# Kernel tuning notes

Measured on AMD Instinct MI355X. Metric: run time of the kernel, lower is better.

Reference implementation:

```python
import jax, jax.numpy as jnp
import numpy as np

EPS = 1e-8
B, N, K, UNITS, FDIMS = 4, 20000, 8, 64, 64
S = K + 1

def _norm(x):
    # euclidean norm over last axis with safe (zero) gradient at 0, same forward as tf.norm
    s = jnp.sum(x * x, axis=-1, keepdims=True)
    return jnp.where(s == 0, 0.0, jnp.sqrt(jnp.where(s == 0, 1.0, s)))

def _conv1d(x, w, b):
    # x: (B,N,S,Cin), w: (3,Cin,Cout); keras Conv1D(kernel=3, padding='same') over the S (1+K) axis + relu
    Bx, Nx, Sx, C = x.shape
    y = jax.lax.conv_general_dilated(x.reshape(Bx * Nx, Sx, C), w, (1,), 'SAME',
                                     dimension_numbers=('NWC', 'WIO', 'NWC'))
    return jax.nn.relu(y + b).reshape(Bx, Nx, Sx, -1)

def _encode(x, ws, bs):
    # encode() from source: channel-sum residual pre-add, then residual loop
    r = _conv1d(x + jnp.sum(x, -1, keepdims=True), ws[0], bs[0])
    for w, b in zip(ws[1:], bs[1:]):
        r = r + _conv1d(r + jnp.sum(r, -1, keepdims=True), w, b)
    return r

def setup_inputs():
    key = jax.random.key(0)
    ks = jax.random.split(key, 32)
    it = iter(list(ks))
    def w(shape, k):
        fan_in = shape[-2] * (shape[0] if len(shape) == 3 else 1)
        return (jax.random.normal(k, shape, jnp.float32) / np.float32(np.sqrt(fan_in)))
    inp = {
        'pc': jax.random.normal(next(it), (B, N, S, 4), jnp.float32),
        'feats': jax.random.normal(next(it), (B, N, S, FDIMS), jnp.float32),
    }
    for name, cin in (('pos', 2), ('rel', 2), ('nrm', 1), ('ang', 3)):
        inp[name + '_w0'] = w((3, cin, UNITS), next(it)); inp[name + '_b0'] = jnp.zeros((UNITS,), jnp.float32)
        inp[name + '_w1'] = w((3, UNITS, UNITS), next(it)); inp[name + '_b1'] = jnp.zeros((UNITS,), jnp.float32)
        inp[name + '_w2'] = w((3, UNITS, UNITS), next(it)); inp[name + '_b2'] = jnp.zeros((UNITS,), jnp.float32)
    inp['mlp_w'] = w((2 * UNITS, UNITS), next(it)); inp['mlp_b'] = jnp.zeros((UNITS,), jnp.float32)
    return inp

def reference(pc, feats, pos_w0, pos_b0, pos_w1, pos_b1, pos_w2, pos_b2,
              rel_w0, rel_b0, rel_w1, rel_b1, rel_w2, rel_b2,
              nrm_w0, nrm_b0, nrm_w1, nrm_b1, nrm_w2, nrm_b2,
              ang_w0, ang_b0, ang_w1, ang_b1, ang_w2, ang_b2,
              mlp_w, mlp_b):
    current = pc[:, :, :1]                          # (B,N,1,4)
    diff = current[..., :2] - pc[..., :2]           # (B,N,S,2)
    norms = _norm(pc[..., :2])                      # (B,N,S,1)
    diff_norm = _norm(diff)
    current_norm = _norm(current)                   # norm over all 4 channels, as in source
    num = jnp.sum(diff * current[..., 2:4], axis=-1, keepdims=True)
    den = diff_norm * current_norm + EPS
    angles = 1.0 - jnp.abs(num / den)
    rppe = jnp.concatenate([pc, diff, norms, angles], axis=-1)  # (B,N,S,8)
    pos, rel_pos = rppe[..., :2], rppe[..., 2:4]
    nrm_in, ang_in = rppe[..., 4:5], rppe[..., 5:]  # faithful to source slicing
    pos_e = _encode(pos, [pos_w0, pos_w1, pos_w2], [pos_b0, pos_b1, pos_b2])
    rel_e = _encode(rel_pos, [rel_w0, rel_w1, rel_w2], [rel_b0, rel_b1, rel_b2])
    nrm_e = _encode(nrm_in, [nrm_w0, nrm_w1, nrm_w2], [nrm_b0, nrm_b1, nrm_b2])
    ang_e = _encode(ang_in, [ang_w0, ang_w1, ang_w2], [ang_b0, ang_b1, ang_b2])
    _ = (pos_e, rel_e)  # computed in the source graph but not used in the output
    r = jax.nn.relu(jnp.einsum('bnsc,co->bnso', jnp.concatenate([nrm_e, ang_e], -1), mlp_w) + mlp_b)
    return jnp.concatenate([r, feats], axis=-1)     # (B,N,S,UNITS+FDIMS)
```

## Files before the change

kernel.cpp:

```cpp
#include <hip/hip_runtime.h>

typedef _Float16 f16;
typedef f16 half4 __attribute__((ext_vector_type(4)));
typedef f16 half8 __attribute__((ext_vector_type(8)));
typedef float f32x4 __attribute__((ext_vector_type(4)));

#define Pv 80000
#define G 7
#define AST 72
#define NROW (G*10+1)
#define NGRP 11429


__global__ void setup_frags(const float* __restrict__ aw0, const float* __restrict__ nw0,
                            const float* __restrict__ aw1, const float* __restrict__ aw2,
                            const float* __restrict__ nw1, const float* __restrict__ nw2,
                            const float* __restrict__ mlp_w, f16* __restrict__ ws)
{
  int tid = blockIdx.x*blockDim.x + threadIdx.x;
  if (tid < 7168){
    int L    = tid / 1792;
    int rem  = tid % 1792;
    int q    = (rem % 448) / 64;
    int lane = rem % 64;
    int nt   = rem / 448;
    const float* W = (L==0)?aw1:(L==1)?aw2:(L==2)?nw1:nw2;
    int n = nt*16 + (lane & 15);
    f16 o8[8];
    #pragma unroll
    for (int j=0;j<8;j++){
      int k = q*32 + (lane>>4)*8 + j;
      float v = 0.f;
      if (k < 192) v = W[k*64 + n];
      else if (k < 195){ int tap = k-192; float s=0.f;
        for (int c=0;c<64;c++) s += W[(tap*64+c)*64 + n]; v = s; }
      o8[j] = (f16)v;
    }
    *(half8*)(ws + (size_t)tid*8) = *(half8*)o8;
  } else if (tid < 8192){
    int t2 = tid - 7168;
    int lane = t2 % 64;
    int q    = (t2 / 64) % 4;
    int nt   = t2 / 256;
    int n = nt*16 + (lane & 15);
    f16 o8[8];
    #pragma unroll
    for (int j=0;j<8;j++){
      int k = q*32 + (lane>>4)*8 + j;
      o8[j] = (f16)mlp_w[k*64 + n];
    }
    *(half8*)(ws + 57344 + (size_t)t2*8) = *(half8*)o8;
  } else if (tid < 8704){
    int t3   = tid - 8192;
    int lane = t3 & 63;
    int nt   = (t3 >> 6) & 3;
    bool isang = t3 < 256;
    int n  = nt*16 + (lane & 15);
    int qd = lane >> 4;
    f16 o8[8];
    #pragma unroll
    for (int j=0;j<8;j++){
      int k = qd*8 + j;
      float v = 0.f;
      if (isang){
        if (k < 9){ int tap = k/3, c = k%3;
          float s3 = aw0[(tap*3+0)*64+n] + aw0[(tap*3+1)*64+n] + aw0[(tap*3+2)*64+n];
          v = aw0[(tap*3+c)*64+n] + s3; }
      } else {
        if (k < 3) v = 2.f * nw0[k*64+n];
      }
      o8[j] = (f16)v;
    }
    *(half8*)(ws + (isang ? 65536 : 67584) + ((size_t)(nt*64+lane))*8) = *(half8*)o8;
  }
}

template<bool IS_ANG>
__device__ __forceinline__ void layer0_mfma(const f16* __restrict__ frag,
    const float* __restrict__ bias, f16* A, int lane, int h, half4 (&cres)[2][4])
{
  const int lo = lane & 15, qd = lane >> 4;
  float bn[4];
  #pragma unroll
  for (int nt=0;nt<4;nt++) bn[nt] = bias[nt*16 + lo];
  f32x4 acc[2][4];
  #pragma unroll
  for (int tt=0;tt<2;tt++)
    #pragma unroll
    for (int nt=0;nt<4;nt++) acc[tt][nt] = (f32x4){bn[nt],bn[nt],bn[nt],bn[nt]};

  half8 bv[4];
  #pragma unroll
  for (int nt=0;nt<4;nt++) bv[nt] = *(const half8*)(frag + ((nt*64+lane))*8);

  const f16 Z = (f16)0;
  #pragma unroll
  for (int tt=0;tt<2;tt++){
    int m = (2*h+tt)*16 + lo; if (m > 62) m = 62;
    int p = m/9, s = m - 9*p;
    const f16* ibp = A + (p*10 + s)*AST + 68;
    half4 h0 = *(const half4*)(ibp);
    half4 h1 = *(const half4*)(ibp + AST);
    half4 h2 = *(const half4*)(ibp + 2*AST);
    half8 av = (half8){Z,Z,Z,Z,Z,Z,Z,Z};
    if (IS_ANG){
      if (qd == 0)      av = (half8){h0[1],h0[2],h0[3],h1[1],h1[2],h1[3],h2[1],h2[2]};
      else if (qd == 1) av = (half8){h2[3],Z,Z,Z,Z,Z,Z,Z};
    } else {
      if (qd == 0)      av = (half8){h0[0],h1[0],h2[0],Z,Z,Z,Z,Z};
    }
    #pragma unroll
    for (int nt=0;nt<4;nt++)
      acc[tt][nt] = __builtin_amdgcn_mfma_f32_16x16x32_f16(av, bv[nt], acc[tt][nt], 0, 0, 0);
  }
  #pragma unroll
  for (int tt=0;tt<2;tt++){
    #pragma unroll
    for (int r=0;r<4;r++){
      int mr = (2*h+tt)*16 + qd*4 + r;
      int mc = mr > 62 ? 62 : mr;
      int pr = mc/9, sr = mc - 9*pr;
      bool vld = (mr < 63);
      f16* rowA = A + (pr*10 + 1 + sr)*AST;
      float tmp = 0.f;
      #pragma unroll
      for (int nt=0;nt<4;nt++){
        float v = fmaxf(acc[tt][nt][r], 0.f);
        cres[tt][nt][r] = (f16)v; tmp += v;
      }
      tmp += __shfl_xor(tmp, 1); tmp += __shfl_xor(tmp, 2);
      tmp += __shfl_xor(tmp, 4); tmp += __shfl_xor(tmp, 8);
      if (vld){
        #pragma unroll
        for (int nt=0;nt<4;nt++) rowA[nt*16 + lo] = cres[tt][nt][r];
        if (lo == 0) rowA[64] = (f16)tmp;
      }
    }
  }
}

template<bool WRITE_RS, bool CARRY_OUT>
__device__ __forceinline__ void conv_layer(const f16* __restrict__ frag,
    const float* __restrict__ bias, f16* A, int lane, int h, half4 (&cres)[2][4])
{
  const int lo = lane & 15, qd = lane >> 4;
  float bn[4];
  #pragma unroll
  for (int nt=0;nt<4;nt++) bn[nt] = bias[nt*16 + lo];
  f32x4 acc[2][4];
  #pragma unroll
  for (int tt=0;tt<2;tt++)
    #pragma unroll
    for (int nt=0;nt<4;nt++) acc[tt][nt] = (f32x4){bn[nt],bn[nt],bn[nt],bn[nt]};

  int abase[2];
  #pragma unroll
  for (int tt=0;tt<2;tt++){
    int m = (2*h+tt)*16 + lo; if (m > 62) m = 62;
    int p = m/9, s = m - 9*p;
    abase[tt] = ((p*10 + s)*AST)*2 + qd*16;
  }
  #pragma unroll
  for (int q=0;q<7;q++){
    half8 bv[4];
    #pragma unroll
    for (int nt=0;nt<4;nt++)
      bv[nt] = *(const half8*)(frag + ((nt*7 + q)*64 + lane)*8);
    #pragma unroll
    for (int tt=0;tt<2;tt++){
      half8 av;
      if (q < 6){
        av = *(const half8*)((const char*)A + abase[tt] + (q>>1)*(AST*2) + (q&1)*64);
      } else {
        const f16* rp = A + ((abase[tt] >> 1) - qd*8 + 64);
        av = (half8){rp[0], rp[AST], rp[2*AST], (f16)0, (f16)0, (f16)0, (f16)0, (f16)0};
      }
      #pragma unroll
      for (int nt=0;nt<4;nt++)
        acc[tt][nt] = __builtin_amdgcn_mfma_f32_16x16x32_f16(av, bv[nt], acc[tt][nt], 0, 0, 0);
    }
  }
  __syncthreads();
  #pragma unroll
  for (int tt=0;tt<2;tt++){
    #pragma unroll
    for (int r=0;r<4;r++){
      int mr = (2*h+tt)*16 + qd*4 + r;
      int mc = mr > 62 ? 62 : mr;
      int pr = mc/9, sr = mc - 9*pr;
      bool vld = (mr < 63);
      f16* rowA = A + (pr*10 + 1 + sr)*AST;
      float tmp = 0.f, rnew[4];
      #pragma unroll
      for (int nt=0;nt<4;nt++){
        float rold = (float)cres[tt][nt][r];
        float v = fmaxf(acc[tt][nt][r], 0.f) + rold;
        rnew[nt] = v; tmp += v;
        if (CARRY_OUT) cres[tt][nt][r] = (f16)v;
      }
      if (WRITE_RS){
        tmp += __shfl_xor(tmp, 1); tmp += __shfl_xor(tmp, 2);
        tmp += __shfl_xor(tmp, 4); tmp += __shfl_xor(tmp, 8);
      }
      if (vld){
        #pragma unroll
        for (int nt=0;nt<4;nt++) rowA[nt*16 + lo] = (f16)rnew[nt];
        if (WRITE_RS && lo == 0) rowA[64] = (f16)tmp;
      }
    }
  }
}

__device__ __forceinline__ void mlp_out(const f16* __restrict__ frag,
    const float* __restrict__ mb, const f16* __restrict__ An, const f16* __restrict__ Aa,
    int lane, int wid, long pbase, float* __restrict__ out)
{
  const int lo = lane & 15, qd = lane >> 4;
  float bn[4];
  #pragma unroll
  for (int nt=0;nt<4;nt++) bn[nt] = mb[nt*16 + lo];
  f32x4 acc[4];
  #pragma unroll
  for (int nt=0;nt<4;nt++) acc[nt] = (f32x4){bn[nt],bn[nt],bn[nt],bn[nt]};

  int m = wid*16 + lo; if (m > 62) m = 62;
  int p = m/9, s = m - 9*p;
  const int aA = ((p*10 + 1 + s)*AST)*2 + qd*16;
  #pragma unroll
  for (int q=0;q<4;q++){
    half8 bv[4];
    #pragma unroll
    for (int nt=0;nt<4;nt++)
      bv[nt] = *(const half8*)(frag + ((nt*4 + q)*64 + lane)*8);
    half8 av = (q < 2)
      ? *(const half8*)((const char*)An + aA + q*64)
      : *(const half8*)((const char*)Aa + aA + (q-2)*64);
    #pragma unroll
    for (int nt=0;nt<4;nt++)
      acc[nt] = __builtin_amdgcn_mfma_f32_16x16x32_f16(av, bv[nt], acc[nt], 0, 0, 0);
  }
  #pragma unroll
  for (int r=0;r<4;r++){
    int mr = wid*16 + qd*4 + r;
    int mc = mr > 62 ? 62 : mr;
    int pr = mc/9, sr = mc - 9*pr;
    long pg = pbase + pr;
    if (mr < 63 && pg < Pv){
      float* op = out + ((long)(pg*9 + sr))*128 + lo;
      #pragma unroll
      for (int nt=0;nt<4;nt++) op[nt*16] = fmaxf(acc[nt][r], 0.f);
    }
  }
}

__global__ __launch_bounds__(256, 3) void locse_main(
    const float* __restrict__ pc, const float* __restrict__ feats,
    const float* __restrict__ nb0, const float* __restrict__ nb1,
    const float* __restrict__ nb2, const float* __restrict__ ab0,
    const float* __restrict__ ab1, const float* __restrict__ ab2,
    const float* __restrict__ mb,  const f16* __restrict__ frag,
    float* __restrict__ out)
{
  __shared__ __align__(16) f16 A2[2][NROW*AST];
  const int tid  = threadIdx.x;
  const int wid  = tid >> 6, lane = tid & 63;
  const int enc  = wid >> 1, h = wid & 1;
  const long pbase = (long)blockIdx.x * G;
  f16* Aw = A2[enc];

  {
    const half8 z8 = {(f16)0,(f16)0,(f16)0,(f16)0,(f16)0,(f16)0,(f16)0,(f16)0};
    for (int i = tid; i < 2*NROW*AST/8; i += 256) ((half8*)A2)[i] = z8;
  }
  if (tid < 63){
    int p = tid/9, s = tid - 9*p;
    long pg = pbase + p;
    if (pg < Pv){
      const float4 v  = *(const float4*)(pc + (pg*9 + s)*4);
      const float4 cu = *(const float4*)(pc + (pg*9)*4);
      float d0 = cu.x - v.x, d1 = cu.y - v.y;
      float n2  = v.x*v.x + v.y*v.y;                        float nrm = n2  > 0.f ? sqrtf(n2)  : 0.f;
      float dn2 = d0*d0 + d1*d1;                            float dn  = dn2 > 0.f ? sqrtf(dn2) : 0.f;
      float cn2 = cu.x*cu.x + cu.y*cu.y + cu.z*cu.z + cu.w*cu.w;
      float cn  = cn2 > 0.f ? sqrtf(cn2) : 0.f;
      float ang = 1.f - fabsf((d0*cu.z + d1*cu.w) / (dn*cn + 1e-8f));
      half4 hv = (half4){(f16)d0, (f16)d1, (f16)nrm, (f16)ang};
      int off = (p*10 + 1 + s)*AST + 68;
      *(half4*)(&A2[0][off]) = hv;
      *(half4*)(&A2[1][off]) = hv;
    }
  }
  __syncthreads();

  const f16*  frag0 = frag + (enc ? 67584 : 65536);
  const float* b0   = enc ? nb0 : ab0;
  const f16*  fragL1= frag + (enc ? 2 : 0)*14336;
  const float* b1   = enc ? nb1 : ab1;
  const f16*  fragL2= frag + (enc ? 3 : 1)*14336;
  const float* b2   = enc ? nb2 : ab2;

  half4 cres[2][4];
  if (enc == 0) layer0_mfma<true >(frag0, b0, Aw, lane, h, cres);
  else          layer0_mfma<false>(frag0, b0, Aw, lane, h, cres);
  __syncthreads();
  conv_layer<true ,true >(fragL1, b1, Aw, lane, h, cres);
  __syncthreads();
  conv_layer<false,false>(fragL2, b2, Aw, lane, h, cres);
  __syncthreads();
  mlp_out(frag + 57344, mb, A2[1], A2[0], lane, wid, pbase, out);

  {
    const float4* ff = (const float4*)feats + pbase*144;
    float4* op = (float4*)out;
    #pragma unroll 1
    for (int i=0;i<4;i++){
      int idx = i*256 + tid;
      if (idx < G*9*16){
        int ps = idx >> 4, c4 = idx & 15;
        long pg = pbase + ps/9;
        if (pg < Pv)
          op[(pbase*9 + (long)ps)*32 + 16 + c4] = ff[(long)ps*16 + c4];
      }
    }
  }
}

extern "C" void kernel_launch(void* const* d_in, const int* in_sizes, int n_in,
                              void* d_out, int out_size, void* d_ws, size_t ws_size,
                              hipStream_t stream)
{
  const float* pc    = (const float*)d_in[0];
  const float* feats = (const float*)d_in[1];
  const float* nw0=(const float*)d_in[14]; const float* nb0=(const float*)d_in[15];
  const float* nw1=(const float*)d_in[16]; const float* nb1=(const float*)d_in[17];
  const float* nw2=(const float*)d_in[18]; const float* nb2=(const float*)d_in[19];
  const float* aw0=(const float*)d_in[20]; const float* ab0=(const float*)d_in[21];
  const float* aw1=(const float*)d_in[22]; const float* ab1=(const float*)d_in[23];
  const float* aw2=(const float*)d_in[24]; const float* ab2=(const float*)d_in[25];
  const float* mw =(const float*)d_in[26]; const float* mb =(const float*)d_in[27];
  f16* ws  = (f16*)d_ws;
  float* out = (float*)d_out;

  setup_frags<<<34, 256, 0, stream>>>(aw0, nw0, aw1, aw2, nw1, nw2, mw, ws);
  locse_main<<<NGRP, 256, 0, stream>>>(pc, feats, nb0, nb1, nb2,
                                       ab0, ab1, ab2, mb, ws, out);
}
```

Measured before the change: 704.7 us.

## Ping-pong LDS activation buffers and prefetch feats into registers early

Each encoder now has two LDS activation buffers, so each conv layer reads from one and writes to the other. This removes the barrier between the MFMA reads and the residual writes inside each conv layer. The feats passthrough is loaded into registers at kernel start, so its global latency overlaps the compute. In exchange, LDS use doubles, which may reduce occupancy below the 3 blocks per CU requested by the launch bounds, and register pressure rises.

```diff
diff --git a/kernel.cpp b/kernel.cpp
--- a/kernel.cpp
+++ b/kernel.cpp
@@ -141,7 +141,8 @@
 
 template<bool WRITE_RS, bool CARRY_OUT>
 __device__ __forceinline__ void conv_layer(const f16* __restrict__ frag,
-    const float* __restrict__ bias, f16* A, int lane, int h, half4 (&cres)[2][4])
+    const float* __restrict__ bias, const f16* __restrict__ Asrc, f16* __restrict__ Adst,
+    int lane, int h, half4 (&cres)[2][4])
 {
   const int lo = lane & 15, qd = lane >> 4;
   float bn[4];
@@ -170,9 +171,9 @@
     for (int tt=0;tt<2;tt++){
       half8 av;
       if (q < 6){
-        av = *(const half8*)((const char*)A + abase[tt] + (q>>1)*(AST*2) + (q&1)*64);
+        av = *(const half8*)((const char*)Asrc + abase[tt] + (q>>1)*(AST*2) + (q&1)*64);
       } else {
-        const f16* rp = A + ((abase[tt] >> 1) - qd*8 + 64);
+        const f16* rp = Asrc + ((abase[tt] >> 1) - qd*8 + 64);
         av = (half8){rp[0], rp[AST], rp[2*AST], (f16)0, (f16)0, (f16)0, (f16)0, (f16)0};
       }
       #pragma unroll
@@ -180,7 +181,6 @@
         acc[tt][nt] = __builtin_amdgcn_mfma_f32_16x16x32_f16(av, bv[nt], acc[tt][nt], 0, 0, 0);
     }
   }
-  __syncthreads();
   #pragma unroll
   for (int tt=0;tt<2;tt++){
     #pragma unroll
@@ -189,7 +189,7 @@
       int mc = mr > 62 ? 62 : mr;
       int pr = mc/9, sr = mc - 9*pr;
       bool vld = (mr < 63);
-      f16* rowA = A + (pr*10 + 1 + sr)*AST;
+      f16* rowD = Adst + (pr*10 + 1 + sr)*AST;
       float tmp = 0.f, rnew[4];
       #pragma unroll
       for (int nt=0;nt<4;nt++){
@@ -204,8 +204,8 @@
       }
       if (vld){
         #pragma unroll
-        for (int nt=0;nt<4;nt++) rowA[nt*16 + lo] = (f16)rnew[nt];
-        if (WRITE_RS && lo == 0) rowA[64] = (f16)tmp;
+        for (int nt=0;nt<4;nt++) rowD[nt*16 + lo] = (f16)rnew[nt];
+        if (WRITE_RS && lo == 0) rowD[64] = (f16)tmp;
       }
     }
   }
@@ -261,17 +261,31 @@
     const float* __restrict__ mb,  const f16* __restrict__ frag,
     float* __restrict__ out)
 {
-  __shared__ __align__(16) f16 A2[2][NROW*AST];
+  __shared__ __align__(16) f16 A4[2][2][NROW*AST];
   const int tid  = threadIdx.x;
   const int wid  = tid >> 6, lane = tid & 63;
   const int enc  = wid >> 1, h = wid & 1;
   const long pbase = (long)blockIdx.x * G;
-  f16* Aw = A2[enc];
+
+  float4 fr[4];
+  {
+    const float4* ff = (const float4*)feats + pbase*144;
+    #pragma unroll
+    for (int i=0;i<4;i++){
+      int idx = i*256 + tid;
+      int ps = idx >> 4, c4 = idx & 15;
+      long pg = pbase + ps/9;
+      fr[i] = (idx < G*9*16 && pg < Pv) ? ff[(long)ps*16 + c4]
+                                        : (float4){0.f,0.f,0.f,0.f};
+    }
+  }
 
   {
     const half8 z8 = {(f16)0,(f16)0,(f16)0,(f16)0,(f16)0,(f16)0,(f16)0,(f16)0};
-    for (int i = tid; i < 2*NROW*AST/8; i += 256) ((half8*)A2)[i] = z8;
-  }
+    for (int i = tid; i < 4*NROW*AST/8; i += 256) ((half8*)A4)[i] = z8;
+  }
+  __syncthreads();
+
   if (tid < 63){
     int p = tid/9, s = tid - 9*p;
     long pg = pbase + p;
@@ -286,8 +300,8 @@
       float ang = 1.f - fabsf((d0*cu.z + d1*cu.w) / (dn*cn + 1e-8f));
       half4 hv = (half4){(f16)d0, (f16)d1, (f16)nrm, (f16)ang};
       int off = (p*10 + 1 + s)*AST + 68;
-      *(half4*)(&A2[0][off]) = hv;
-      *(half4*)(&A2[1][off]) = hv;
+      *(half4*)(&A4[0][0][off]) = hv;
+      *(half4*)(&A4[1][0][off]) = hv;
     }
   }
   __syncthreads();
@@ -298,28 +312,29 @@
   const float* b1   = enc ? nb1 : ab1;
   const f16*  fragL2= frag + (enc ? 3 : 1)*14336;
   const float* b2   = enc ? nb2 : ab2;
+  f16* B0 = A4[enc][0];
+  f16* B1 = A4[enc][1];
 
   half4 cres[2][4];
-  if (enc == 0) layer0_mfma<true >(frag0, b0, Aw, lane, h, cres);
-  else          layer0_mfma<false>(frag0, b0, Aw, lane, h, cres);
-  __syncthreads();
-  conv_layer<true ,true >(fragL1, b1, Aw, lane, h, cres);
-  __syncthreads();
-  conv_layer<false,false>(fragL2, b2, Aw, lane, h, cres);
-  __syncthreads();
-  mlp_out(frag + 57344, mb, A2[1], A2[0], lane, wid, pbase, out);
+  if (enc == 0) layer0_mfma<true >(frag0, b0, B0, lane, h, cres);
+  else          layer0_mfma<false>(frag0, b0, B0, lane, h, cres);
+  __syncthreads();
+  conv_layer<true ,true >(fragL1, b1, B0, B1, lane, h, cres);
+  __syncthreads();
+  conv_layer<false,false>(fragL2, b2, B1, B0, lane, h, cres);
+  __syncthreads();
+  mlp_out(frag + 57344, mb, A4[1][0], A4[0][0], lane, wid, pbase, out);
 
   {
-    const float4* ff = (const float4*)feats + pbase*144;
     float4* op = (float4*)out;
-    #pragma unroll 1
+    #pragma unroll
     for (int i=0;i<4;i++){
       int idx = i*256 + tid;
       if (idx < G*9*16){
         int ps = idx >> 4, c4 = idx & 15;
         long pg = pbase + ps/9;
         if (pg < Pv)
-          op[(pbase*9 + (long)ps)*32 + 16 + c4] = ff[(long)ps*16 + c4];
+          op[(pbase*9 + (long)ps)*32 + 16 + c4] = fr[i];
       }
     }
   }
```

New measurement: 755.2 us. 1.07x slower.
